# Optimization experiments

Measured on AMD Instinct MI355X. Metric: run time of the kernel, lower is better.

The kernel has to match this reference:

```python
import jax, jax.numpy as jnp
import numpy as np

B, L, H, NH = 1, 4096, 768, 12
HD = H // NH  # 64


def setup_inputs() -> dict:
    key = jax.random.key(0)
    ks = jax.random.split(key, 10)
    inp = {
        "query": jax.random.normal(ks[0], (B, L, H), jnp.float32),
        "key": jax.random.normal(ks[1], (B, L, H), jnp.float32),
        "value": jax.random.normal(ks[2], (B, L, H), jnp.float32),
        "attention_mask": jnp.zeros((B, 1, 1, L), jnp.float32),
        # learned params (nn.Linear: y = x @ W.T + b)
        "Wq": jax.random.normal(ks[3], (H, H), jnp.float32) * 0.02,
        "bq": jnp.zeros((H,), jnp.float32),
        "Wk": jax.random.normal(ks[4], (H, H), jnp.float32) * 0.02,
        "bk": jnp.zeros((H,), jnp.float32),
        "Wv": jax.random.normal(ks[5], (H, H), jnp.float32) * 0.02,
        "bv": jnp.zeros((H,), jnp.float32),
    }
    return inp


def _split_heads(x):
    # [B, L, H] -> [B, NH, L, HD]
    b, l, _ = x.shape
    return x.reshape(b, l, NH, HD).transpose(0, 2, 1, 3)


def reference(query, key, value, attention_mask, Wq, bq, Wk, bk, Wv, bv):
    q = _split_heads(query @ Wq.T + bq)   # [B, NH, Lq, HD]
    k = _split_heads(key @ Wk.T + bk)     # [B, NH, Lk, HD]
    v = _split_heads(value @ Wv.T + bv)   # [B, NH, Lk, HD]

    scale = 1.0 / jnp.sqrt(jnp.asarray(HD, q.dtype))
    scores = jnp.einsum("bhqd,bhkd->bhqk", q, k) * scale
    scores = scores + attention_mask  # additive mask, broadcasts over heads/queries
    probs = jax.nn.softmax(scores, axis=-1)
    # dropout is identity in eval mode (reference baseline)
    ctx = jnp.einsum("bhqk,bhkd->bhqd", probs, v)  # [B, NH, Lq, HD]
    out = ctx.transpose(0, 2, 1, 3).reshape(query.shape[0], query.shape[1], H)
    return out
```

## Files before the change

### kernel.cpp

```cpp
#include <hip/hip_runtime.h>
#include <math.h>

#define LSEQ 4096
#define HDIM 768
#define NHEAD 12

using v4f    = __attribute__((ext_vector_type(4))) float;
using short8 = __attribute__((ext_vector_type(8))) short;
using u32x4  = __attribute__((ext_vector_type(4))) unsigned int;

#if __has_builtin(__builtin_amdgcn_exp2f)
#define EXP2F(x) __builtin_amdgcn_exp2f(x)
#else
#define EXP2F(x) exp2f(x)
#endif

__device__ __forceinline__ unsigned short f2bf(float f) {
  union { float f; unsigned u; } v; v.f = f;
  unsigned r = v.u + 0x7fffu + ((v.u >> 16) & 1u);
  return (unsigned short)(r >> 16);
}

__device__ __forceinline__ short8 ld8(const float* p, size_t off) {
  const float* f = p + off;
  float t[8];
  *(u32x4*)&t[0] = *(const u32x4*)(f);
  *(u32x4*)&t[4] = *(const u32x4*)(f + 4);
  short8 r;
#pragma unroll
  for (int i = 0; i < 8; ++i) r[i] = (short)f2bf(t[i]);
  return r;
}

__global__ __launch_bounds__(256, 2) void proj_gemm(
    const float* __restrict__ Xq, const float* __restrict__ Xk,
    const float* __restrict__ Xv,
    const float* __restrict__ Wq, const float* __restrict__ Wk,
    const float* __restrict__ Wv,
    const float* __restrict__ bq, const float* __restrict__ bk,
    const float* __restrict__ bv,
    unsigned short* __restrict__ dst_base)
{
  __shared__ __align__(16) unsigned short a_lds[128 * 32];
  __shared__ __align__(16) unsigned short b_lds[128 * 32];
  __shared__ __align__(16) unsigned short c_lds[64 * 136];

  const int z = blockIdx.z;
  const float* X = (z == 0) ? Xq : ((z == 1) ? Xk : Xv);
  const float* W = (z == 0) ? Wq : ((z == 1) ? Wk : Wv);
  const float* bias = (z == 0) ? bq : ((z == 1) ? bk : bv);
  unsigned short* dst = dst_base + (size_t)z * NHEAD * LSEQ * 64;

  const int tid = threadIdx.x;
  const int wave = tid >> 6, lane = tid & 63;
  const int quad = lane >> 4, l16 = lane & 15;
  const int wm = (wave >> 1) * 64, wn = (wave & 1) * 64;
  const int bm = blockIdx.y * 128, bn = blockIdx.x * 128;

  v4f acc[4][4];
  for (int i = 0; i < 4; ++i)
    for (int j = 0; j < 4; ++j)
      acc[i][j] = (v4f){0.f, 0.f, 0.f, 0.f};

  const int row_s = tid >> 2;
  const int c8_s = (tid & 3) * 8;

  for (int k0 = 0; k0 < HDIM; k0 += 32) {
    __syncthreads();
    for (int s = 0; s < 2; ++s) {
      int row = row_s + s * 64;
      *(short8*)&a_lds[row * 32 + c8_s] = ld8(X, (size_t)(bm + row) * HDIM + k0 + c8_s);
      *(short8*)&b_lds[row * 32 + c8_s] = ld8(W, (size_t)(bn + row) * HDIM + k0 + c8_s);
    }
    __syncthreads();

    short8 af[4], bfr[4];
    for (int i = 0; i < 4; ++i)
      af[i] = *(const short8*)&a_lds[(wm + i * 16 + l16) * 32 + quad * 8];
    for (int j = 0; j < 4; ++j)
      bfr[j] = *(const short8*)&b_lds[(wn + j * 16 + l16) * 32 + quad * 8];
    if (z == 2) {
      for (int i = 0; i < 4; ++i)
        for (int j = 0; j < 4; ++j)
          acc[i][j] = __builtin_amdgcn_mfma_f32_16x16x32_bf16(bfr[j], af[i], acc[i][j], 0, 0, 0);
    } else {
      for (int i = 0; i < 4; ++i)
        for (int j = 0; j < 4; ++j)
          acc[i][j] = __builtin_amdgcn_mfma_f32_16x16x32_bf16(af[i], bfr[j], acc[i][j], 0, 0, 0);
    }
  }

  for (int p = 0; p < 2; ++p) {
    __syncthreads();
    if (z == 2) {
      if ((wave & 1) == p) {
        for (int j = 0; j < 4; ++j)
          for (int r = 0; r < 4; ++r) {
            float bv = bias[bn + wn + j * 16 + quad * 4 + r];
            int row = j * 16 + quad * 4 + r;
            for (int i = 0; i < 4; ++i)
              c_lds[row * 136 + wm + i * 16 + l16] = f2bf(acc[i][j][r] + bv);
          }
      }
    } else {
      if ((wave >> 1) == p) {
        for (int j = 0; j < 4; ++j) {
          float bv = bias[bn + wn + j * 16 + l16];
          for (int i = 0; i < 4; ++i)
            for (int r = 0; r < 4; ++r)
              c_lds[(i * 16 + quad * 4 + r) * 136 + wn + j * 16 + l16] =
                  f2bf(acc[i][j][r] + bv);
        }
      }
    }
    __syncthreads();
    int row = tid >> 2, c = tid & 3;
    const unsigned short* srow = &c_lds[row * 136 + c * 32];
    if (z == 2) {
      int n = bn + p * 64 + row;
      int hh = n >> 6, d = n & 63;
      unsigned short* drow = dst + ((size_t)hh * 64 + d) * LSEQ + bm + c * 32;
      for (int q8 = 0; q8 < 4; ++q8)
        *(u32x4*)(drow + q8 * 8) = *(const u32x4*)(srow + q8 * 8);
    } else {
      int m = bm + p * 64 + row;
      int nbase = bn + c * 32;
      int hh = nbase >> 6, d = nbase & 63;
      unsigned short* drow = dst + ((size_t)hh * LSEQ + m) * 64 + d;
      for (int q8 = 0; q8 < 4; ++q8)
        *(u32x4*)(drow + q8 * 8) = *(const u32x4*)(srow + q8 * 8);
    }
  }
}

__global__ __launch_bounds__(256, 3) void attn(
    const unsigned short* __restrict__ Q, const unsigned short* __restrict__ K,
    const unsigned short* __restrict__ Vt, const float* __restrict__ mask,
    float* __restrict__ out)
{
  __shared__ __align__(16) unsigned short k_lds[128 * 64];
  __shared__ __align__(16) unsigned short vt_lds[64 * 128];
  __shared__ __align__(16) unsigned short p_lds[4][16 * 128];

  const int h = blockIdx.y;
  const int qt = blockIdx.x;
  const int tid = threadIdx.x;
  const int wave = tid >> 6, lane = tid & 63;
  const int quad = lane >> 4, l16 = lane & 15;

  const unsigned short* Qh  = Q  + (size_t)h * LSEQ * 64;
  const unsigned short* Kh  = K  + (size_t)h * LSEQ * 64;
  const unsigned short* Vth = Vt + (size_t)h * 64 * LSEQ;

  const int qrow = qt * 64 + wave * 16;
  short8 qf[2];
  for (int c = 0; c < 2; ++c)
    qf[c] = *(const short8*)(Qh + (size_t)(qrow + l16) * 64 + c * 32 + quad * 8);

  v4f acc_o[4];
  for (int j = 0; j < 4; ++j) acc_o[j] = (v4f){0.f, 0.f, 0.f, 0.f};
  float lsum[4] = {0.f, 0.f, 0.f, 0.f};

  for (int kt = 0; kt < 32; ++kt) {
    const int key0 = kt * 128;

    float mk[8];
#pragma unroll
    for (int j = 0; j < 8; ++j) mk[j] = mask[key0 + j * 16 + l16] * 1.44269504f;

    __syncthreads();
#pragma unroll
    for (int s = 0; s < 4; ++s) {
      int ch = tid + 256 * s;
      int row = ch >> 3, c8 = ch & 7;
      *(u32x4*)&k_lds[row * 64 + ((c8 ^ (row & 7)) << 3)] =
          *(const u32x4*)(Kh + (size_t)(key0 + row) * 64 + c8 * 8);
    }
#pragma unroll
    for (int s = 0; s < 4; ++s) {
      int ch = tid + 256 * s;
      int d = ch >> 4, kb = ch & 15;
      *(u32x4*)&vt_lds[d * 128 + ((kb ^ (d & 7)) << 3)] =
          *(const u32x4*)(Vth + (size_t)d * LSEQ + key0 + kb * 8);
    }
    __syncthreads();

    v4f sacc[8];
#pragma unroll
    for (int j = 0; j < 8; ++j) sacc[j] = (v4f){0.f, 0.f, 0.f, 0.f};
#pragma unroll
    for (int c = 0; c < 2; ++c)
#pragma unroll
      for (int j = 0; j < 8; ++j) {
        int row = j * 16 + l16;
        short8 kf = *(const short8*)&k_lds[row * 64 + (((c * 4 + quad) ^ (row & 7)) << 3)];
        sacc[j] = __builtin_amdgcn_mfma_f32_16x16x32_bf16(qf[c], kf, sacc[j], 0, 0, 0);
      }

#pragma unroll
    for (int j = 0; j < 8; ++j) {
#pragma unroll
      for (int r = 0; r < 4; ++r) {
        union { float f; unsigned u; } pu;
        pu.f = EXP2F(fmaf(sacc[j][r], 0.18033688f, mk[j]));
        pu.u &= 0xffff0000u;
        lsum[r] += pu.f;
        int row = quad * 4 + r, col = j * 16 + l16;
        p_lds[wave][row * 128 + (((col >> 3) ^ (row & 7)) << 3) + (col & 7)] =
            (unsigned short)(pu.u >> 16);
      }
    }
    short8 pf[4];
#pragma unroll
    for (int c = 0; c < 4; ++c)
      pf[c] = *(const short8*)&p_lds[wave][l16 * 128 + (((c * 4 + quad) ^ (l16 & 7)) << 3)];

#pragma unroll
    for (int kk = 0; kk < 4; ++kk)
#pragma unroll
      for (int j = 0; j < 4; ++j) {
        int d = j * 16 + l16;
        short8 vf = *(const short8*)&vt_lds[d * 128 + (((kk * 4 + quad) ^ (d & 7)) << 3)];
        acc_o[j] = __builtin_amdgcn_mfma_f32_16x16x32_bf16(pf[kk], vf, acc_o[j], 0, 0, 0);
      }
  }

  for (int r = 0; r < 4; ++r) {
    float s = lsum[r];
    for (int off = 8; off; off >>= 1) s += __shfl_xor(s, off, 64);
    lsum[r] = s;
  }

  for (int j = 0; j < 4; ++j) {
    int col = h * 64 + j * 16 + l16;
    for (int r = 0; r < 4; ++r) {
      int row = qt * 64 + wave * 16 + quad * 4 + r;
      out[(size_t)row * HDIM + col] = acc_o[j][r] / lsum[r];
    }
  }
}

extern "C" void kernel_launch(void* const* d_in, const int* in_sizes, int n_in,
                              void* d_out, int out_size, void* d_ws, size_t ws_size,
                              hipStream_t stream) {
  const float* query = (const float*)d_in[0];
  const float* key   = (const float*)d_in[1];
  const float* value = (const float*)d_in[2];
  const float* mask  = (const float*)d_in[3];
  const float* Wq = (const float*)d_in[4];
  const float* bq = (const float*)d_in[5];
  const float* Wk = (const float*)d_in[6];
  const float* bk = (const float*)d_in[7];
  const float* Wv = (const float*)d_in[8];
  const float* bv = (const float*)d_in[9];
  float* out = (float*)d_out;

  unsigned short* Qb = (unsigned short*)d_ws;
  unsigned short* Kb = Qb + (size_t)NHEAD * LSEQ * 64;
  unsigned short* Vb = Kb + (size_t)NHEAD * LSEQ * 64;

  proj_gemm<<<dim3(HDIM / 128, LSEQ / 128, 3), 256, 0, stream>>>(
      query, key, value, Wq, Wk, Wv, bq, bk, bv, Qb);
  attn<<<dim3(LSEQ / 64, NHEAD), 256, 0, stream>>>(Qb, Kb, Vb, mask, out);
}
```

Before: 255.6 us.

## Prefetch next tiles into registers in both kernels and remap GEMM blocks per XCD

Both the projection GEMM and the attention kernel now load the next K/V (or X/W) tile from global memory into registers while the current tile is being computed, then write it to LDS after the barrier. This hides global-load latency behind MFMA work, at the cost of extra registers. The GEMM grid is flattened to 1D and remapped so that blocks sharing the same X row-panel land on the same XCD, which should improve L2 reuse. The P-tile LDS swizzle is also changed to cut bank conflicts on the probability writes.

```diff
diff --git a/kernel.cpp b/kernel.cpp
--- a/kernel.cpp
+++ b/kernel.cpp
@@ -21,14 +21,18 @@
   return (unsigned short)(r >> 16);
 }
 
-__device__ __forceinline__ short8 ld8(const float* p, size_t off) {
-  const float* f = p + off;
-  float t[8];
-  *(u32x4*)&t[0] = *(const u32x4*)(f);
-  *(u32x4*)&t[4] = *(const u32x4*)(f + 4);
+__device__ __forceinline__ short8 cvt8(u32x4 a, u32x4 b) {
   short8 r;
 #pragma unroll
-  for (int i = 0; i < 8; ++i) r[i] = (short)f2bf(t[i]);
+  for (int i = 0; i < 4; ++i) {
+    unsigned u = a[i];
+    r[i] = (short)((u + 0x7fffu + ((u >> 16) & 1u)) >> 16);
+  }
+#pragma unroll
+  for (int i = 0; i < 4; ++i) {
+    unsigned u = b[i];
+    r[4 + i] = (short)((u + 0x7fffu + ((u >> 16) & 1u)) >> 16);
+  }
   return r;
 }
 
@@ -45,7 +49,13 @@
   __shared__ __align__(16) unsigned short b_lds[128 * 32];
   __shared__ __align__(16) unsigned short c_lds[64 * 136];
 
-  const int z = blockIdx.z;
+  const int id = blockIdx.x;
+  const int xcd = id & 7, local = id >> 3;
+  const int grp = local / 6, bnIdx = local % 6;
+  const int G = grp * 8 + xcd;
+  const int z = G >> 5;
+  const int bm = (G & 31) * 128, bn = bnIdx * 128;
+
   const float* X = (z == 0) ? Xq : ((z == 1) ? Xk : Xv);
   const float* W = (z == 0) ? Wq : ((z == 1) ? Wk : Wv);
   const float* bias = (z == 0) ? bq : ((z == 1) ? bk : bv);
@@ -55,7 +65,6 @@
   const int wave = tid >> 6, lane = tid & 63;
   const int quad = lane >> 4, l16 = lane & 15;
   const int wm = (wave >> 1) * 64, wn = (wave & 1) * 64;
-  const int bm = blockIdx.y * 128, bn = blockIdx.x * 128;
 
   v4f acc[4][4];
   for (int i = 0; i < 4; ++i)
@@ -65,14 +74,38 @@
   const int row_s = tid >> 2;
   const int c8_s = (tid & 3) * 8;
 
+  const float* xrow[2]; const float* wrow[2];
+#pragma unroll
+  for (int s = 0; s < 2; ++s) {
+    xrow[s] = X + (size_t)(bm + row_s + 64 * s) * HDIM + c8_s;
+    wrow[s] = W + (size_t)(bn + row_s + 64 * s) * HDIM + c8_s;
+  }
+
+  u32x4 pa[2][2], pb[2][2];
+#pragma unroll
+  for (int s = 0; s < 2; ++s) {
+    pa[s][0] = *(const u32x4*)(xrow[s]);     pa[s][1] = *(const u32x4*)(xrow[s] + 4);
+    pb[s][0] = *(const u32x4*)(wrow[s]);     pb[s][1] = *(const u32x4*)(wrow[s] + 4);
+  }
+
   for (int k0 = 0; k0 < HDIM; k0 += 32) {
     __syncthreads();
+#pragma unroll
     for (int s = 0; s < 2; ++s) {
-      int row = row_s + s * 64;
-      *(short8*)&a_lds[row * 32 + c8_s] = ld8(X, (size_t)(bm + row) * HDIM + k0 + c8_s);
-      *(short8*)&b_lds[row * 32 + c8_s] = ld8(W, (size_t)(bn + row) * HDIM + k0 + c8_s);
-    }
-    __syncthreads();
+      *(short8*)&a_lds[(row_s + 64 * s) * 32 + c8_s] = cvt8(pa[s][0], pa[s][1]);
+      *(short8*)&b_lds[(row_s + 64 * s) * 32 + c8_s] = cvt8(pb[s][0], pb[s][1]);
+    }
+    __syncthreads();
+
+    if (k0 + 32 < HDIM) {
+#pragma unroll
+      for (int s = 0; s < 2; ++s) {
+        pa[s][0] = *(const u32x4*)(xrow[s] + k0 + 32);
+        pa[s][1] = *(const u32x4*)(xrow[s] + k0 + 36);
+        pb[s][0] = *(const u32x4*)(wrow[s] + k0 + 32);
+        pb[s][1] = *(const u32x4*)(wrow[s] + k0 + 36);
+      }
+    }
 
     short8 af[4], bfr[4];
     for (int i = 0; i < 4; ++i)
@@ -96,20 +129,20 @@
       if ((wave & 1) == p) {
         for (int j = 0; j < 4; ++j)
           for (int r = 0; r < 4; ++r) {
-            float bv = bias[bn + wn + j * 16 + quad * 4 + r];
+            float bvv = bias[bn + wn + j * 16 + quad * 4 + r];
             int row = j * 16 + quad * 4 + r;
             for (int i = 0; i < 4; ++i)
-              c_lds[row * 136 + wm + i * 16 + l16] = f2bf(acc[i][j][r] + bv);
+              c_lds[row * 136 + wm + i * 16 + l16] = f2bf(acc[i][j][r] + bvv);
           }
       }
     } else {
       if ((wave >> 1) == p) {
         for (int j = 0; j < 4; ++j) {
-          float bv = bias[bn + wn + j * 16 + l16];
+          float bvv = bias[bn + wn + j * 16 + l16];
           for (int i = 0; i < 4; ++i)
             for (int r = 0; r < 4; ++r)
               c_lds[(i * 16 + quad * 4 + r) * 136 + wn + j * 16 + l16] =
-                  f2bf(acc[i][j][r] + bv);
+                  f2bf(acc[i][j][r] + bvv);
         }
       }
     }
@@ -152,6 +185,28 @@
   const unsigned short* Kh  = K  + (size_t)h * LSEQ * 64;
   const unsigned short* Vth = Vt + (size_t)h * 64 * LSEQ;
 
+  const unsigned short* kptr[4]; const unsigned short* vptr[4];
+  unsigned short* kdst[4]; unsigned short* vdst[4];
+#pragma unroll
+  for (int s = 0; s < 4; ++s) {
+    int ch = tid + 256 * s;
+    int krow = ch >> 3, kc8 = ch & 7;
+    kptr[s] = Kh + (size_t)krow * 64 + kc8 * 8;
+    kdst[s] = &k_lds[krow * 64 + ((kc8 ^ (krow & 7)) << 3)];
+    int d = ch >> 4, kb = ch & 15;
+    vptr[s] = Vth + (size_t)d * LSEQ + kb * 8;
+    vdst[s] = &vt_lds[d * 128 + ((kb ^ (d & 7)) << 3)];
+  }
+
+  int pswzW[4];
+#pragma unroll
+  for (int r = 0; r < 4; ++r) {
+    int row = quad * 4 + r;
+    pswzW[r] = (row ^ (row >> 2)) & 7;
+  }
+  const int pswzR = (l16 ^ (l16 >> 2)) & 7;
+  const int phi = l16 >> 3, plo = l16 & 7;
+
   const int qrow = qt * 64 + wave * 16;
   short8 qf[2];
   for (int c = 0; c < 2; ++c)
@@ -161,28 +216,22 @@
   for (int j = 0; j < 4; ++j) acc_o[j] = (v4f){0.f, 0.f, 0.f, 0.f};
   float lsum[4] = {0.f, 0.f, 0.f, 0.f};
 
+  u32x4 kreg[4], vreg[4];
+  float mk[8];
+#pragma unroll
+  for (int s = 0; s < 4; ++s) {
+    kreg[s] = *(const u32x4*)(kptr[s]);
+    vreg[s] = *(const u32x4*)(vptr[s]);
+  }
+#pragma unroll
+  for (int j = 0; j < 8; ++j) mk[j] = mask[j * 16 + l16] * 1.44269504f;
+
   for (int kt = 0; kt < 32; ++kt) {
-    const int key0 = kt * 128;
-
-    float mk[8];
-#pragma unroll
-    for (int j = 0; j < 8; ++j) mk[j] = mask[key0 + j * 16 + l16] * 1.44269504f;
-
-    __syncthreads();
-#pragma unroll
-    for (int s = 0; s < 4; ++s) {
-      int ch = tid + 256 * s;
-      int row = ch >> 3, c8 = ch & 7;
-      *(u32x4*)&k_lds[row * 64 + ((c8 ^ (row & 7)) << 3)] =
-          *(const u32x4*)(Kh + (size_t)(key0 + row) * 64 + c8 * 8);
-    }
-#pragma unroll
-    for (int s = 0; s < 4; ++s) {
-      int ch = tid + 256 * s;
-      int d = ch >> 4, kb = ch & 15;
-      *(u32x4*)&vt_lds[d * 128 + ((kb ^ (d & 7)) << 3)] =
-          *(const u32x4*)(Vth + (size_t)d * LSEQ + key0 + kb * 8);
-    }
+    __syncthreads();
+#pragma unroll
+    for (int s = 0; s < 4; ++s) *(u32x4*)kdst[s] = kreg[s];
+#pragma unroll
+    for (int s = 0; s < 4; ++s) *(u32x4*)vdst[s] = vreg[s];
     __syncthreads();
 
     v4f sacc[8];
@@ -196,6 +245,18 @@
         short8 kf = *(const short8*)&k_lds[row * 64 + (((c * 4 + quad) ^ (row & 7)) << 3)];
         sacc[j] = __builtin_amdgcn_mfma_f32_16x16x32_bf16(qf[c], kf, sacc[j], 0, 0, 0);
       }
+
+    float mknext[8];
+    if (kt < 31) {
+      size_t ko = (size_t)(kt + 1) * 8192, vo = (size_t)(kt + 1) * 128;
+#pragma unroll
+      for (int s = 0; s < 4; ++s) {
+        kreg[s] = *(const u32x4*)(kptr[s] + ko);
+        vreg[s] = *(const u32x4*)(vptr[s] + vo);
+      }
+#pragma unroll
+      for (int j = 0; j < 8; ++j) mknext[j] = mask[(kt + 1) * 128 + j * 16 + l16];
+    }
 
 #pragma unroll
     for (int j = 0; j < 8; ++j) {
@@ -205,15 +266,14 @@
         pu.f = EXP2F(fmaf(sacc[j][r], 0.18033688f, mk[j]));
         pu.u &= 0xffff0000u;
         lsum[r] += pu.f;
-        int row = quad * 4 + r, col = j * 16 + l16;
-        p_lds[wave][row * 128 + (((col >> 3) ^ (row & 7)) << 3) + (col & 7)] =
+        p_lds[wave][(quad * 4 + r) * 128 + (((2 * j + phi) ^ pswzW[r]) << 3) + plo] =
             (unsigned short)(pu.u >> 16);
       }
     }
     short8 pf[4];
 #pragma unroll
     for (int c = 0; c < 4; ++c)
-      pf[c] = *(const short8*)&p_lds[wave][l16 * 128 + (((c * 4 + quad) ^ (l16 & 7)) << 3)];
+      pf[c] = *(const short8*)&p_lds[wave][l16 * 128 + (((c * 4 + quad) ^ pswzR) << 3)];
 
 #pragma unroll
     for (int kk = 0; kk < 4; ++kk)
@@ -223,6 +283,11 @@
         short8 vf = *(const short8*)&vt_lds[d * 128 + (((kk * 4 + quad) ^ (d & 7)) << 3)];
         acc_o[j] = __builtin_amdgcn_mfma_f32_16x16x32_bf16(pf[kk], vf, acc_o[j], 0, 0, 0);
       }
+
+    if (kt < 31) {
+#pragma unroll
+      for (int j = 0; j < 8; ++j) mk[j] = mknext[j] * 1.44269504f;
+    }
   }
 
   for (int r = 0; r < 4; ++r) {
@@ -259,7 +324,7 @@
   unsigned short* Kb = Qb + (size_t)NHEAD * LSEQ * 64;
   unsigned short* Vb = Kb + (size_t)NHEAD * LSEQ * 64;
 
-  proj_gemm<<<dim3(HDIM / 128, LSEQ / 128, 3), 256, 0, stream>>>(
+  proj_gemm<<<576, 256, 0, stream>>>(
       query, key, value, Wq, Wk, Wv, bq, bk, bv, Qb);
   attn<<<dim3(LSEQ / 64, NHEAD), 256, 0, stream>>>(Qb, Kb, Vb, mask, out);
 }
```

Result: slower. 382.4 us (+49.6%).
